# Optimization experiments

Measured on AMD Instinct MI355X. Metric: run time of the kernel, lower is better.

The kernel has to match this reference:

```python
import jax, jax.numpy as jnp
import numpy as np

D_MODEL = 256
NEG_INF = -1e9  # matches masked_fill value in the torch module


def setup_inputs() -> dict:
    key = jax.random.key(0)
    ks = jax.random.split(key, 7)
    B, S, D = 4, 4096, D_MODEL
    enc_q = jax.random.normal(ks[0], (B, S, D), dtype=jnp.float32)
    enc_k = jax.random.normal(ks[1], (B, S, D), dtype=jnp.float32)
    enc_v = jax.random.normal(ks[2], (B, S, D), dtype=jnp.float32)
    mask = jax.random.randint(ks[3], (B, S, S), 0, 2).astype(jnp.bool_)
    scale = 1.0 / np.sqrt(D)
    W_q = jax.random.normal(ks[4], (D, D), dtype=jnp.float32) * scale
    W_k = jax.random.normal(ks[5], (D, D), dtype=jnp.float32) * scale
    W_v = jax.random.normal(ks[6], (D, D), dtype=jnp.float32) * scale
    return {"encodings_q": enc_q, "encodings_k": enc_k, "encodings_v": enc_v,
            "mask": mask, "W_q": W_q, "W_k": W_k, "W_v": W_v}


def reference(encodings_q, encodings_k, encodings_v, mask, W_q, W_k, W_v):
    # nn.Linear(bias=False): y = x @ W^T
    q = jnp.einsum('bsd,ed->bse', encodings_q, W_q)
    k = jnp.einsum('bsd,ed->bse', encodings_k, W_k)
    v = jnp.einsum('bsd,ed->bse', encodings_v, W_v)
    sims = jnp.einsum('bqd,bkd->bqk', q, k) / jnp.sqrt(jnp.float32(D_MODEL))
    sims = jnp.where(mask, jnp.float32(NEG_INF), sims)
    attn = jax.nn.softmax(sims, axis=-1)
    return jnp.einsum('bqk,bkd->bqd', attn, v)
```

## Files before the change

kernel.cpp:

```cpp
#include <hip/hip_runtime.h>
#include <hip/hip_bf16.h>
#include <stdint.h>


typedef __attribute__((ext_vector_type(8))) short bf16x8;
typedef __attribute__((ext_vector_type(4))) float f32x4;

__device__ __forceinline__ short f2bf(float f) {
    union { float f; uint32_t u; } v; v.f = f;
    uint32_t r = v.u + 0x7FFFu + ((v.u >> 16) & 1u);
    return (short)(r >> 16);
}
__device__ __forceinline__ float bf2f(short s) {
    union { uint32_t u; float f; } v; v.u = ((uint32_t)(uint16_t)s) << 16;
    return v.f;
}

__global__ __launch_bounds__(512, 2)
void proj_kernel(const float* __restrict__ encq,
                 const float* __restrict__ enck,
                 const float* __restrict__ encv,
                 const float* __restrict__ Wq,
                 const float* __restrict__ Wk,
                 const float* __restrict__ Wv,
                 short* __restrict__ q_out,
                 short* __restrict__ k_out,
                 short* __restrict__ vt_out)
{
    __shared__ short As[128][72];
    __shared__ short Bs[256][72];

    const int tid = threadIdx.x;
    const int wave = tid >> 6, lane = tid & 63, lo = lane & 15, hi = lane >> 4;
    const int proj = blockIdx.y;
    const int row0 = blockIdx.x * 128;

    const float* X = (proj == 0) ? encq : (proj == 1) ? enck : encv;
    const float* W = (proj == 0) ? Wq   : (proj == 1) ? Wk   : Wv;

    f32x4 acc[16];
    #pragma unroll
    for (int n = 0; n < 16; ++n) {
        f32x4 z = {0.f, 0.f, 0.f, 0.f};
        acc[n] = z;
    }

    for (int ks = 0; ks < 4; ++ks) {
        const int k0 = ks * 64;
        __syncthreads();
        #pragma unroll
        for (int i = 0; i < 4; ++i) {
            int u = tid + i * 512;
            int r = u >> 4, c4 = u & 15;
            float4 v = *(const float4*)(X + (size_t)(row0 + r) * 256 + k0 + c4 * 4);
            short* dst = &As[r][c4 * 4];
            dst[0] = f2bf(v.x); dst[1] = f2bf(v.y); dst[2] = f2bf(v.z); dst[3] = f2bf(v.w);
        }
        #pragma unroll
        for (int i = 0; i < 8; ++i) {
            int u = tid + i * 512;
            int r = u >> 4, c4 = u & 15;
            float4 v = *(const float4*)(W + (size_t)r * 256 + k0 + c4 * 4);
            short* dst = &Bs[r][c4 * 4];
            dst[0] = f2bf(v.x); dst[1] = f2bf(v.y); dst[2] = f2bf(v.z); dst[3] = f2bf(v.w);
        }
        __syncthreads();
        #pragma unroll
        for (int kl = 0; kl < 2; ++kl) {
            bf16x8 a = *(const bf16x8*)&As[wave * 16 + lo][kl * 32 + hi * 8];
            #pragma unroll
            for (int n = 0; n < 16; ++n) {
                bf16x8 b = *(const bf16x8*)&Bs[n * 16 + lo][kl * 32 + hi * 8];
                acc[n] = __builtin_amdgcn_mfma_f32_16x16x32_bf16(a, b, acc[n], 0, 0, 0);
            }
        }
    }

    #pragma unroll
    for (int n = 0; n < 16; ++n)
        #pragma unroll
        for (int j = 0; j < 4; ++j) {
            int srow = row0 + wave * 16 + hi * 4 + j;
            int e = n * 16 + lo;
            float v = acc[n][j];
            if (proj == 0) {
                q_out[(size_t)srow * 256 + e] = f2bf(v * 0.0625f);
            } else if (proj == 1) {
                k_out[(size_t)srow * 256 + e] = f2bf(v);
            } else {
                int b = srow >> 12, s = srow & 4095;
                vt_out[((size_t)b * 256 + e) * 4096 + s] = f2bf(v);
            }
        }
}

__global__ __launch_bounds__(512, 2)
void attn_kernel(const short* __restrict__ qs,
                 const short* __restrict__ kk_,
                 const short* __restrict__ vt,
                 const int*   __restrict__ mask,
                 short* __restrict__ Opart,
                 float* __restrict__ Mpart,
                 float* __restrict__ Lpart)
{
    __shared__ short Ks[32 * 256];
    __shared__ short Vs[256 * 32];
    __shared__ short Ps[8][16][40];
    __shared__ unsigned int Mb32[128];

    const int tid = threadIdx.x;
    const int wave = tid >> 6, lane = tid & 63, lo = lane & 15, hi = lane >> 4;
    const int qt = blockIdx.x, b = blockIdx.y, split = blockIdx.z;
    const int qrow0 = qt * 128 + wave * 16;
    const size_t qg0 = (size_t)b * 4096 + qrow0;
    const int kv0 = split * 1024;

    bf16x8 qf[8];
    #pragma unroll
    for (int kk = 0; kk < 8; ++kk)
        qf[kk] = *(const bf16x8*)(qs + (qg0 + lo) * 256 + kk * 32 + hi * 8);

    f32x4 oacc[16];
    #pragma unroll
    for (int n = 0; n < 16; ++n) {
        f32x4 z = {0.f, 0.f, 0.f, 0.f};
        oacc[n] = z;
    }
    float Mst[4], Lst[4];
    #pragma unroll
    for (int j = 0; j < 4; ++j) { Mst[j] = -1e30f; Lst[j] = 0.f; }

    bf16x8 onesf;
    #pragma unroll
    for (int i = 0; i < 8; ++i) onesf[i] = (short)0x3F80;

    const short* ksrc0 = kk_ + ((size_t)b * 4096 + kv0) * 256;
    const size_t vbase = (size_t)b * 256 * 4096;
    const int mrow = tid >> 2, mpart = tid & 3;
    const int* msrc0 = mask + (size_t)b * 4096 * 4096
                     + (size_t)(qt * 128 + mrow) * 4096 + kv0 + mpart * 8;

    bf16x8 kreg[2], vreg[2];
    int4 mreg[2];
    #pragma unroll
    for (int i = 0; i < 2; ++i) {
        int u = tid + i * 512;
        kreg[i] = *(const bf16x8*)(ksrc0 + u * 8);
    }
    #pragma unroll
    for (int i = 0; i < 2; ++i) {
        int u = tid + i * 512;
        int r = u >> 2, cu = u & 3;
        vreg[i] = *(const bf16x8*)(vt + vbase + (size_t)r * 4096 + kv0 + cu * 8);
    }
    #pragma unroll
    for (int i = 0; i < 2; ++i)
        mreg[i] = *(const int4*)(msrc0 + i * 4);

    for (int t = 0; t < 32; ++t) {
        __syncthreads();
        #pragma unroll
        for (int i = 0; i < 2; ++i) {
            int u = tid + i * 512;
            int row = u >> 5, unit = u & 31;
            *(bf16x8*)&Ks[row * 256 + (unit ^ (row & 7)) * 8] = kreg[i];
        }
        #pragma unroll
        for (int i = 0; i < 2; ++i) {
            int u = tid + i * 512;
            int r = u >> 2, cu = u & 3;
            *(bf16x8*)&Vs[r * 32 + (cu ^ (r & 3)) * 8] = vreg[i];
        }
        {
            uint32_t mb = 0;
            #pragma unroll
            for (int i = 0; i < 2; ++i) {
                mb |= (uint32_t)(mreg[i].x != 0) << (i * 4);
                mb |= (uint32_t)(mreg[i].y != 0) << (i * 4 + 1);
                mb |= (uint32_t)(mreg[i].z != 0) << (i * 4 + 2);
                mb |= (uint32_t)(mreg[i].w != 0) << (i * 4 + 3);
            }
            ((unsigned char*)&Mb32[mrow])[mpart] = (unsigned char)mb;
        }
        __syncthreads();

        if (t < 31) {
            const short* src = ksrc0 + (size_t)(t + 1) * 32 * 256;
            #pragma unroll
            for (int i = 0; i < 2; ++i) {
                int u = tid + i * 512;
                kreg[i] = *(const bf16x8*)(src + u * 8);
            }
            const int c0 = kv0 + (t + 1) * 32;
            #pragma unroll
            for (int i = 0; i < 2; ++i) {
                int u = tid + i * 512;
                int r = u >> 2, cu = u & 3;
                vreg[i] = *(const bf16x8*)(vt + vbase + (size_t)r * 4096 + c0 + cu * 8);
            }
            const int* ms = msrc0 + (t + 1) * 32;
            #pragma unroll
            for (int i = 0; i < 2; ++i)
                mreg[i] = *(const int4*)(ms + i * 4);
        }

        uint32_t wls[4];
        #pragma unroll
        for (int j = 0; j < 4; ++j)
            wls[j] = Mb32[wave * 16 + hi * 4 + j] >> lo;

        f32x4 sacc[2];
        #pragma unroll
        for (int n = 0; n < 2; ++n) {
            f32x4 z = {0.f, 0.f, 0.f, 0.f};
            sacc[n] = z;
        }
        #pragma unroll
        for (int kk = 0; kk < 8; ++kk) {
            #pragma unroll
            for (int n = 0; n < 2; ++n) {
                int row = n * 16 + lo;
                bf16x8 bk = *(const bf16x8*)&Ks[row * 256 + ((kk * 4 + hi) ^ (lo & 7)) * 8];
                sacc[n] = __builtin_amdgcn_mfma_f32_16x16x32_bf16(qf[kk], bk, sacc[n], 0, 0, 0);
            }
        }

        float ml[4];
        #pragma unroll
        for (int j = 0; j < 4; ++j) {
            float mx = -1e30f;
            #pragma unroll
            for (int n = 0; n < 2; ++n) {
                float s = sacc[n][j];
                if ((wls[j] >> (n * 16)) & 1u) s = -1e30f;
                mx = fmaxf(mx, s);
            }
            #pragma unroll
            for (int d = 1; d < 16; d <<= 1)
                mx = fmaxf(mx, __shfl_xor(mx, d));
            ml[j] = mx;
        }

        bool needl = false;
        #pragma unroll
        for (int j = 0; j < 4; ++j)
            needl = needl || (ml[j] > Mst[j] + 8.0f);
        if (__any((int)needl)) {
            #pragma unroll
            for (int j = 0; j < 4; ++j) {
                float Mn = fmaxf(Mst[j], ml[j]);
                float sc = __expf(Mst[j] - Mn);
                Mst[j] = Mn;
                Lst[j] *= sc;
                #pragma unroll
                for (int n = 0; n < 16; ++n) oacc[n][j] *= sc;
            }
        }

        #pragma unroll
        for (int n = 0; n < 2; ++n)
            #pragma unroll
            for (int j = 0; j < 4; ++j) {
                float p = __expf(sacc[n][j] - Mst[j]);
                if ((wls[j] >> (n * 16)) & 1u) p = 0.0f;
                Ps[wave][hi * 4 + j][n * 16 + lo] = f2bf(p);
            }
        bf16x8 a2 = *(const bf16x8*)&Ps[wave][lo][hi * 8];
        #pragma unroll
        for (int n = 0; n < 16; ++n) {
            int row = n * 16 + lo;
            bf16x8 bv = *(const bf16x8*)&Vs[row * 32 + (hi ^ (lo & 3)) * 8];
            oacc[n] = __builtin_amdgcn_mfma_f32_16x16x32_bf16(a2, bv, oacc[n], 0, 0, 0);
        }
        f32x4 lacc = __builtin_amdgcn_mfma_f32_16x16x32_bf16(a2, onesf,
                         (f32x4){0.f, 0.f, 0.f, 0.f}, 0, 0, 0);
        #pragma unroll
        for (int j = 0; j < 4; ++j)
            Lst[j] += lacc[j];
    }

    const size_t obase = ((size_t)split * 16384 + qg0) * 256;
    #pragma unroll
    for (int n = 0; n < 16; ++n)
        #pragma unroll
        for (int j = 0; j < 4; ++j)
            Opart[obase + (size_t)(hi * 4 + j) * 256 + n * 16 + lo] = f2bf(oacc[n][j]);
    if (lo == 0) {
        #pragma unroll
        for (int j = 0; j < 4; ++j) {
            size_t r = (size_t)split * 16384 + qg0 + hi * 4 + j;
            Mpart[r] = Mst[j];
            Lpart[r] = Lst[j];
        }
    }
}

__global__ __launch_bounds__(256)
void combine_kernel(const short* __restrict__ Opart,
                    const float* __restrict__ Mpart,
                    const float* __restrict__ Lpart,
                    float* __restrict__ out)
{
    int gid = blockIdx.x * 256 + threadIdx.x;
    int row = gid >> 6, c4 = gid & 63;
    float Ms[4], Ls[4], M = -1e30f;
    #pragma unroll
    for (int sp = 0; sp < 4; ++sp) {
        Ms[sp] = Mpart[sp * 16384 + row];
        Ls[sp] = Lpart[sp * 16384 + row];
        M = fmaxf(M, Ms[sp]);
    }
    float w[4], denom = 0.f;
    #pragma unroll
    for (int sp = 0; sp < 4; ++sp) {
        w[sp] = __expf(Ms[sp] - M);
        denom += w[sp] * Ls[sp];
    }
    float inv = 1.0f / denom;
    float4 r = {0.f, 0.f, 0.f, 0.f};
    #pragma unroll
    for (int sp = 0; sp < 4; ++sp) {
        short4 o = *(const short4*)(Opart + ((size_t)sp * 16384 + row) * 256 + c4 * 4);
        r.x += w[sp] * bf2f(o.x);
        r.y += w[sp] * bf2f(o.y);
        r.z += w[sp] * bf2f(o.z);
        r.w += w[sp] * bf2f(o.w);
    }
    r.x *= inv; r.y *= inv; r.z *= inv; r.w *= inv;
    *(float4*)(out + (size_t)row * 256 + c4 * 4) = r;
}

extern "C" void kernel_launch(void* const* d_in, const int* in_sizes, int n_in,
                              void* d_out, int out_size, void* d_ws, size_t ws_size,
                              hipStream_t stream)
{
    const float* encq = (const float*)d_in[0];
    const float* enck = (const float*)d_in[1];
    const float* encv = (const float*)d_in[2];
    const int*   mask = (const int*)d_in[3];
    const float* Wq   = (const float*)d_in[4];
    const float* Wk   = (const float*)d_in[5];
    const float* Wv   = (const float*)d_in[6];

    char* ws = (char*)d_ws;
    short* q_ws  = (short*)(ws);
    short* k_ws  = (short*)(ws + 8388608);
    short* vt_ws = (short*)(ws + 16777216);
    short* Opart = (short*)(ws + 25165824);
    float* Mpart = (float*)(ws + 58720256);
    float* Lpart = (float*)(ws + 58982400);
    float* out   = (float*)d_out;

    hipLaunchKernelGGL(proj_kernel, dim3(128, 3), dim3(512), 0, stream,
                       encq, enck, encv, Wq, Wk, Wv, q_ws, k_ws, vt_ws);
    hipLaunchKernelGGL(attn_kernel, dim3(32, 4, 4), dim3(512), 0, stream,
                       q_ws, k_ws, vt_ws, mask, Opart, Mpart, Lpart);
    hipLaunchKernelGGL(combine_kernel, dim3(4096), dim3(256), 0, stream,
                       Opart, Mpart, Lpart, out);
}
```

Baseline: 220.0 us.

## Stage K/V directly into LDS with global_load_lds and halve the attention block

The attention kernel now copies K and V tiles straight from global memory into LDS with __builtin_amdgcn_global_load_lds, using a swizzled source address, instead of staging them through registers. The block shrinks from 8 waves to 4 and covers 64 query rows, so the grid doubles and launch bounds become (256, 3). This frees VGPRs and removes the register-to-LDS store instructions. In exchange, the next tile's load is issued after the end-of-iteration barrier and waited on at the next barrier, so load/compute overlap within a block is reduced. Each K/V tile is also fetched by twice as many blocks.

```diff
diff --git a/kernel.cpp b/kernel.cpp
--- a/kernel.cpp
+++ b/kernel.cpp
@@ -94,7 +94,7 @@
         }
 }
 
-__global__ __launch_bounds__(512, 2)
+__global__ __launch_bounds__(256, 3)
 void attn_kernel(const short* __restrict__ qs,
                  const short* __restrict__ kk_,
                  const short* __restrict__ vt,
@@ -105,13 +105,13 @@
 {
     __shared__ short Ks[32 * 256];
     __shared__ short Vs[256 * 32];
-    __shared__ short Ps[8][16][40];
-    __shared__ unsigned int Mb32[128];
+    __shared__ short Ps[4][16][40];
+    __shared__ unsigned int Mb32[64];
 
     const int tid = threadIdx.x;
     const int wave = tid >> 6, lane = tid & 63, lo = lane & 15, hi = lane >> 4;
     const int qt = blockIdx.x, b = blockIdx.y, split = blockIdx.z;
-    const int qrow0 = qt * 128 + wave * 16;
+    const int qrow0 = qt * 64 + wave * 16;
     const size_t qg0 = (size_t)b * 4096 + qrow0;
     const int kv0 = split * 1024;
 
@@ -135,42 +135,39 @@
     for (int i = 0; i < 8; ++i) onesf[i] = (short)0x3F80;
 
     const short* ksrc0 = kk_ + ((size_t)b * 4096 + kv0) * 256;
-    const size_t vbase = (size_t)b * 256 * 4096;
+    const short* vsrc0 = vt + (size_t)b * 256 * 4096;
     const int mrow = tid >> 2, mpart = tid & 3;
     const int* msrc0 = mask + (size_t)b * 4096 * 4096
-                     + (size_t)(qt * 128 + mrow) * 4096 + kv0 + mpart * 8;
-
-    bf16x8 kreg[2], vreg[2];
+                     + (size_t)(qt * 64 + mrow) * 4096 + kv0 + mpart * 8;
+
+    auto stage_kv = [&](int t) {
+        const short* ks = ksrc0 + (size_t)t * 32 * 256;
+        #pragma unroll
+        for (int i = 0; i < 4; ++i) {
+            int c = wave * 4 + i;
+            int s = c * 64 + lane;
+            int row = s >> 5, wa = s & 31;
+            const short* g = ks + row * 256 + ((wa ^ (row & 7)) * 8);
+            __builtin_amdgcn_global_load_lds((const void*)g, (void*)&Ks[c * 512], 16, 0, 0);
+        }
+        const int c0 = kv0 + t * 32;
+        #pragma unroll
+        for (int i = 0; i < 4; ++i) {
+            int c = wave * 4 + i;
+            int s = c * 64 + lane;
+            int r = s >> 2, wa = s & 3;
+            const short* g = vsrc0 + (size_t)r * 4096 + c0 + ((wa ^ (r & 3)) * 8);
+            __builtin_amdgcn_global_load_lds((const void*)g, (void*)&Vs[c * 512], 16, 0, 0);
+        }
+    };
+
     int4 mreg[2];
-    #pragma unroll
-    for (int i = 0; i < 2; ++i) {
-        int u = tid + i * 512;
-        kreg[i] = *(const bf16x8*)(ksrc0 + u * 8);
-    }
-    #pragma unroll
-    for (int i = 0; i < 2; ++i) {
-        int u = tid + i * 512;
-        int r = u >> 2, cu = u & 3;
-        vreg[i] = *(const bf16x8*)(vt + vbase + (size_t)r * 4096 + kv0 + cu * 8);
-    }
+    stage_kv(0);
     #pragma unroll
     for (int i = 0; i < 2; ++i)
         mreg[i] = *(const int4*)(msrc0 + i * 4);
 
     for (int t = 0; t < 32; ++t) {
-        __syncthreads();
-        #pragma unroll
-        for (int i = 0; i < 2; ++i) {
-            int u = tid + i * 512;
-            int row = u >> 5, unit = u & 31;
-            *(bf16x8*)&Ks[row * 256 + (unit ^ (row & 7)) * 8] = kreg[i];
-        }
-        #pragma unroll
-        for (int i = 0; i < 2; ++i) {
-            int u = tid + i * 512;
-            int r = u >> 2, cu = u & 3;
-            *(bf16x8*)&Vs[r * 32 + (cu ^ (r & 3)) * 8] = vreg[i];
-        }
         {
             uint32_t mb = 0;
             #pragma unroll
@@ -183,26 +180,6 @@
             ((unsigned char*)&Mb32[mrow])[mpart] = (unsigned char)mb;
         }
         __syncthreads();
-
-        if (t < 31) {
-            const short* src = ksrc0 + (size_t)(t + 1) * 32 * 256;
-            #pragma unroll
-            for (int i = 0; i < 2; ++i) {
-                int u = tid + i * 512;
-                kreg[i] = *(const bf16x8*)(src + u * 8);
-            }
-            const int c0 = kv0 + (t + 1) * 32;
-            #pragma unroll
-            for (int i = 0; i < 2; ++i) {
-                int u = tid + i * 512;
-                int r = u >> 2, cu = u & 3;
-                vreg[i] = *(const bf16x8*)(vt + vbase + (size_t)r * 4096 + c0 + cu * 8);
-            }
-            const int* ms = msrc0 + (t + 1) * 32;
-            #pragma unroll
-            for (int i = 0; i < 2; ++i)
-                mreg[i] = *(const int4*)(ms + i * 4);
-        }
 
         uint32_t wls[4];
         #pragma unroll
@@ -277,6 +254,16 @@
         #pragma unroll
         for (int j = 0; j < 4; ++j)
             Lst[j] += lacc[j];
+
+        __syncthreads();
+
+        if (t < 31) {
+            stage_kv(t + 1);
+            const int* ms = msrc0 + (t + 1) * 32;
+            #pragma unroll
+            for (int i = 0; i < 2; ++i)
+                mreg[i] = *(const int4*)(ms + i * 4);
+        }
     }
 
     const size_t obase = ((size_t)split * 16384 + qg0) * 256;
@@ -353,7 +340,7 @@
 
     hipLaunchKernelGGL(proj_kernel, dim3(128, 3), dim3(512), 0, stream,
                        encq, enck, encv, Wq, Wk, Wv, q_ws, k_ws, vt_ws);
-    hipLaunchKernelGGL(attn_kernel, dim3(32, 4, 4), dim3(512), 0, stream,
+    hipLaunchKernelGGL(attn_kernel, dim3(64, 4, 4), dim3(256), 0, stream,
                        q_ws, k_ws, vt_ws, mask, Opart, Mpart, Lpart);
     hipLaunchKernelGGL(combine_kernel, dim3(4096), dim3(256), 0, stream,
                        Opart, Mpart, Lpart, out);
```

Result: slower. 281.7 us (+28.1%).
